# Kernel optimization log

Measured on AMD Instinct MI355X. Metric: run time of the kernel, lower is better.

The kernel has to match this reference:

```python
import jax, jax.numpy as jnp
import numpy as np

B, S, H, D = 8, 4096, 1024, 256  # batch, seq, hidden_size, state_size


def setup_inputs() -> dict:
    key = jax.random.key(0)
    ks = jax.random.split(key, 4)
    scale_in = 1.0 / np.sqrt(H)
    scale_st = 1.0 / np.sqrt(D)
    return {
        "x": jax.random.normal(ks[0], (B, S, H), dtype=jnp.float32),
        "W_in": jax.random.normal(ks[1], (H, D), dtype=jnp.float32) * scale_in,
        "b_in": jnp.zeros((D,), dtype=jnp.float32),
        "W_state": jax.random.normal(ks[2], (D, D), dtype=jnp.float32) * scale_st,
        "b_state": jnp.zeros((D,), dtype=jnp.float32),
        "W_out": jax.random.normal(ks[3], (D, H), dtype=jnp.float32) * scale_st,
        "b_out": jnp.zeros((H,), dtype=jnp.float32),
    }


def reference(x, W_in, b_in, W_state, b_state, W_out, b_out):
    # Precompute input projection for all timesteps in one big GEMM: [B,S,D]
    inp = jnp.einsum("bsh,hd->bsd", x, W_in) + b_in

    def step(state, inp_t):
        # state: [B,D], inp_t: [B,D]
        state = jnp.tanh(inp_t + state @ W_state + b_state)
        return state, state

    state0 = jnp.zeros((x.shape[0], W_state.shape[0]), dtype=x.dtype)
    # scan over time axis -> states: [S,B,D]
    _, states = jax.lax.scan(step, state0, jnp.swapaxes(inp, 0, 1))
    # output projection: [S,B,H] -> [B,S,H]
    out = jnp.einsum("sbd,dh->sbh", states, W_out) + b_out
    return jnp.swapaxes(out, 0, 1)
```

## Files before the change

### kernel.cpp

```cpp
#include <hip/hip_runtime.h>


typedef float v4f __attribute__((ext_vector_type(4)));
typedef __bf16 bf16x4 __attribute__((ext_vector_type(4)));
typedef __bf16 bf16x8 __attribute__((ext_vector_type(8)));
typedef _Float16 h8 __attribute__((ext_vector_type(8)));

#define BARRIER_LGKM() asm volatile("s_waitcnt lgkmcnt(0)\n\ts_barrier" ::: "memory")

__global__ void cvt_f32_bf16_x4(const float* __restrict__ in,
                                __bf16* __restrict__ out, int n4) {
  int i = blockIdx.x * blockDim.x + threadIdx.x;
  if (i >= n4) return;
  v4f v = ((const v4f*)in)[i];
  bf16x4 o;
  o.x = (__bf16)v.x; o.y = (__bf16)v.y; o.z = (__bf16)v.z; o.w = (__bf16)v.w;
  ((bf16x4*)out)[i] = o;
}

__global__ void transpose_cvt(const float* __restrict__ in,
                              __bf16* __restrict__ out, int K, int N) {
  int i = blockIdx.x * blockDim.x + threadIdx.x;
  if (i >= K * N) return;
  int k = i / N;
  int n = i - k * N;
  out[(size_t)n * K + k] = (__bf16)in[i];
}

__global__ void gemm_bt(const __bf16* __restrict__ A,
                        const __bf16* __restrict__ Bt,
                        const float* __restrict__ bias,
                        float* __restrict__ C,
                        int M, int N, int K) {
  int wid  = (blockIdx.x * blockDim.x + threadIdx.x) >> 6;
  int lane = threadIdx.x & 63;
  int ntiles = N >> 4;
  int mt = wid / ntiles;
  int nt = wid - mt * ntiles;
  if (mt * 16 >= M) return;
  int r = lane & 15;
  int q = lane >> 4;
  const __bf16* arow = A + (size_t)(mt * 16 + r) * K + q * 8;
  const __bf16* brow = Bt + (size_t)(nt * 16 + r) * K + q * 8;
  v4f acc = {0.f, 0.f, 0.f, 0.f};
  for (int k = 0; k < K; k += 32) {
    bf16x8 af = *(const bf16x8*)(arow + k);
    bf16x8 bf = *(const bf16x8*)(brow + k);
    acc = __builtin_amdgcn_mfma_f32_16x16x32_bf16(af, bf, acc, 0, 0, 0);
  }
  int col = nt * 16 + r;
  float bv = bias[col];
  size_t base = (size_t)(mt * 16 + q * 4) * N + col;
#pragma unroll
  for (int i = 0; i < 4; ++i) C[base + (size_t)i * N] = acc[i] + bv;
}

__global__ __launch_bounds__(256, 1) void scan_mfma(
    const float* __restrict__ inp,
    const float* __restrict__ Wst,
    const float* __restrict__ b_state,
    __bf16* __restrict__ states,
    int S) {
  const int tid = threadIdx.x;
  const int l = tid & 63;
  const int q = l >> 4;
  const int r = l & 15;
  const int w = tid >> 6;
  const int b = blockIdx.x;

  __shared__ __align__(16) _Float16 sbuf[2][256];

  h8 bw0[8], bw1[8], bw2[8], bw3[8];
#pragma unroll
  for (int c = 0; c < 8; ++c) {
#pragma unroll
    for (int i = 0; i < 8; ++i) {
      const float* wr = Wst + (size_t)(32 * c + 8 * q + i) * 256 + w * 64 + r;
      bw0[c][i] = (_Float16)wr[0];
      bw1[c][i] = (_Float16)wr[16];
      bw2[c][i] = (_Float16)wr[32];
      bw3[c][i] = (_Float16)wr[48];
    }
  }

  const float bst = b_state[tid];
  const float* inpb = inp + (size_t)b * S * 256;
  __bf16* stb = states + (size_t)b * S * 256;

  sbuf[0][tid] = (_Float16)0.f;
  float u_cur = inpb[tid];
  float u_nxt = inpb[256 + tid];
  __syncthreads();

  int cur = 0;
  for (int t = 0; t < S; ++t) {
    float u_n2 = 0.f;
    if (t + 2 < S) u_n2 = inpb[(size_t)(t + 2) * 256 + tid];

    const h8* sp = (const h8*)sbuf[cur];
    h8 af[8];
#pragma unroll
    for (int c = 0; c < 8; ++c) af[c] = sp[4 * c + q];

    v4f a0 = {0.f, 0.f, 0.f, 0.f};
    v4f a1 = a0, a2 = a0, a3 = a0;
#pragma unroll
    for (int c = 0; c < 8; ++c) {
      a0 = __builtin_amdgcn_mfma_f32_16x16x32_f16(af[c], bw0[c], a0, 0, 0, 0);
      a1 = __builtin_amdgcn_mfma_f32_16x16x32_f16(af[c], bw1[c], a1, 0, 0, 0);
      a2 = __builtin_amdgcn_mfma_f32_16x16x32_f16(af[c], bw2[c], a2, 0, 0, 0);
      a3 = __builtin_amdgcn_mfma_f32_16x16x32_f16(af[c], bw3[c], a3, 0, 0, 0);
    }
    float x = (q == 0) ? a0[0] : (q == 1) ? a1[0] : (q == 2) ? a2[0] : a3[0];
    x += u_cur + bst;

    float e = __expf(2.f * x);
    float sn = 1.f - 2.f * __builtin_amdgcn_rcpf(e + 1.f);

    cur ^= 1;
    sbuf[cur][tid] = (_Float16)sn;
    stb[(size_t)t * 256 + tid] = (__bf16)sn;
    u_cur = u_nxt;
    u_nxt = u_n2;
    BARRIER_LGKM();
  }
}

extern "C" void kernel_launch(void* const* d_in, const int* in_sizes, int n_in,
                              void* d_out, int out_size, void* d_ws,
                              size_t ws_size, hipStream_t stream) {
  const float* x       = (const float*)d_in[0];
  const float* W_in    = (const float*)d_in[1];
  const float* b_in    = (const float*)d_in[2];
  const float* W_state = (const float*)d_in[3];
  const float* b_state = (const float*)d_in[4];
  const float* W_out   = (const float*)d_in[5];
  const float* b_out   = (const float*)d_in[6];
  float* out = (float*)d_out;

  const int B = 8, S = 4096, H = 1024, D = 256;
  const int M = B * S;

  char* ws = (char*)d_ws;
  float*  inp    = (float*)(ws + 0);
  __bf16* states = (__bf16*)(ws + 33554432);
  __bf16* xb     = (__bf16*)(ws + 50331648);
  __bf16* WinT   = (__bf16*)(ws + 117440512);
  __bf16* WoutT  = (__bf16*)(ws + 117964800);

  cvt_f32_bf16_x4<<<(M * H / 4 + 255) / 256, 256, 0, stream>>>(x, xb, M * H / 4);
  transpose_cvt<<<(H * D + 255) / 256, 256, 0, stream>>>(W_in, WinT, H, D);
  transpose_cvt<<<(D * H + 255) / 256, 256, 0, stream>>>(W_out, WoutT, D, H);

  {
    int waves = (M / 16) * (D / 16);
    gemm_bt<<<waves / 4, 256, 0, stream>>>(xb, WinT, b_in, inp, M, D, H);
  }

  scan_mfma<<<B, 256, 0, stream>>>(inp, W_state, b_state, states, S);

  {
    int waves = (M / 16) * (H / 16);
    gemm_bt<<<waves / 4, 256, 0, stream>>>(states, WoutT, b_out, out, M, H, D);
  }
}
```

Baseline: 2.621 ms.

## Replace per-wave GEMM with LDS-tiled double-buffered 128x128 MFMA GEMM

The naive GEMM, where each wave computes one 16x16 tile straight from global memory, is replaced by a 128x128 block-tiled kernel. It stages A and B tiles into swizzled LDS using global_load_lds and double-buffers them across the K loop, so operands are reused across 16 MFMA accumulators per wave. The scan loop also gets small tweaks: pointer-increment addressing, an exp2f-based tanh, and removal of the t+2 bounds check. That last change reads past the end of each batch's input on the final steps, which still lands inside the workspace.

```diff
diff --git a/kernel.cpp b/kernel.cpp
--- a/kernel.cpp
+++ b/kernel.cpp
@@ -1,4 +1,5 @@
 #include <hip/hip_runtime.h>
+#include <stdint.h>
 
 
 typedef float v4f __attribute__((ext_vector_type(4)));
@@ -7,6 +8,11 @@
 typedef _Float16 h8 __attribute__((ext_vector_type(8)));
 
 #define BARRIER_LGKM() asm volatile("s_waitcnt lgkmcnt(0)\n\ts_barrier" ::: "memory")
+
+#define GLOAD_LDS16(g, l)                                                    \
+  __builtin_amdgcn_global_load_lds(                                          \
+      (const __attribute__((address_space(1))) void*)(g),                    \
+      (__attribute__((address_space(3))) void*)(l), 16, 0, 0)
 
 __global__ void cvt_f32_bf16_x4(const float* __restrict__ in,
                                 __bf16* __restrict__ out, int n4) {
@@ -27,32 +33,99 @@
   out[(size_t)n * K + k] = (__bf16)in[i];
 }
 
-__global__ void gemm_bt(const __bf16* __restrict__ A,
-                        const __bf16* __restrict__ Bt,
-                        const float* __restrict__ bias,
-                        float* __restrict__ C,
-                        int M, int N, int K) {
-  int wid  = (blockIdx.x * blockDim.x + threadIdx.x) >> 6;
-  int lane = threadIdx.x & 63;
-  int ntiles = N >> 4;
-  int mt = wid / ntiles;
-  int nt = wid - mt * ntiles;
-  if (mt * 16 >= M) return;
-  int r = lane & 15;
-  int q = lane >> 4;
-  const __bf16* arow = A + (size_t)(mt * 16 + r) * K + q * 8;
-  const __bf16* brow = Bt + (size_t)(nt * 16 + r) * K + q * 8;
-  v4f acc = {0.f, 0.f, 0.f, 0.f};
-  for (int k = 0; k < K; k += 32) {
-    bf16x8 af = *(const bf16x8*)(arow + k);
-    bf16x8 bf = *(const bf16x8*)(brow + k);
-    acc = __builtin_amdgcn_mfma_f32_16x16x32_bf16(af, bf, acc, 0, 0, 0);
-  }
-  int col = nt * 16 + r;
-  float bv = bias[col];
-  size_t base = (size_t)(mt * 16 + q * 4) * N + col;
-#pragma unroll
-  for (int i = 0; i < 4; ++i) C[base + (size_t)i * N] = acc[i] + bv;
+__global__ __launch_bounds__(256) void gemm_tile(
+    const __bf16* __restrict__ A,
+    const __bf16* __restrict__ Bt,
+    const float* __restrict__ bias,
+    float* __restrict__ C,
+    int M, int N, int K) {
+  const int tid = threadIdx.x;
+  const int lane = tid & 63;
+  const int w = tid >> 6;
+  const int wr = w >> 1, wc = w & 1;
+  const int r = lane & 15, q = lane >> 4;
+
+  const int nbn = N >> 7;
+  const int mb = blockIdx.x / nbn;
+  const int nb = blockIdx.x - mb * nbn;
+  const int m0 = mb << 7, n0 = nb << 7;
+
+  __shared__ __align__(16) char lds[2][16384];
+
+  const __bf16* gA[2];
+  const __bf16* gB[2];
+  int loff[2];
+#pragma unroll
+  for (int j = 0; j < 2; ++j) {
+    int o = (w * 2 + j) * 1024 + lane * 16;
+    int row = o >> 6;
+    int s = (o >> 4) & 3;
+    int ss = s ^ ((row >> 1) & 3);
+    gA[j] = A + (size_t)(m0 + row) * K + ss * 8;
+    gB[j] = Bt + (size_t)(n0 + row) * K + ss * 8;
+    loff[j] = (w * 2 + j) * 1024;
+  }
+
+  const int slot = (q ^ ((r >> 1) & 3)) * 16;
+  int aoff[4], boff[4];
+#pragma unroll
+  for (int i = 0; i < 4; ++i) {
+    aoff[i] = (wr * 64 + i * 16 + r) * 64 + slot;
+    boff[i] = 8192 + (wc * 64 + i * 16 + r) * 64 + slot;
+  }
+
+  v4f acc[4][4];
+#pragma unroll
+  for (int mi = 0; mi < 4; ++mi)
+#pragma unroll
+    for (int ni = 0; ni < 4; ++ni) acc[mi][ni] = (v4f){0.f, 0.f, 0.f, 0.f};
+
+  const int NK = K >> 5;
+#pragma unroll
+  for (int j = 0; j < 2; ++j) {
+    GLOAD_LDS16(gA[j], lds[0] + loff[j]);
+    GLOAD_LDS16(gB[j], lds[0] + 8192 + loff[j]);
+  }
+
+  for (int kt = 0; kt < NK; ++kt) {
+    __syncthreads();
+    if (kt + 1 < NK) {
+      const int b = (kt + 1) & 1;
+      const int ke = (kt + 1) * 32;
+#pragma unroll
+      for (int j = 0; j < 2; ++j) {
+        GLOAD_LDS16(gA[j] + ke, lds[b] + loff[j]);
+        GLOAD_LDS16(gB[j] + ke, lds[b] + 8192 + loff[j]);
+      }
+    }
+    const char* Lb = lds[kt & 1];
+    bf16x8 af[4], bf[4];
+#pragma unroll
+    for (int i = 0; i < 4; ++i) af[i] = *(const bf16x8*)(Lb + aoff[i]);
+#pragma unroll
+    for (int i = 0; i < 4; ++i) bf[i] = *(const bf16x8*)(Lb + boff[i]);
+#pragma unroll
+    for (int mi = 0; mi < 4; ++mi)
+#pragma unroll
+      for (int ni = 0; ni < 4; ++ni)
+        acc[mi][ni] = __builtin_amdgcn_mfma_f32_16x16x32_bf16(
+            af[mi], bf[ni], acc[mi][ni], 0, 0, 0);
+  }
+
+  float bv[4];
+#pragma unroll
+  for (int ni = 0; ni < 4; ++ni) bv[ni] = bias[n0 + wc * 64 + ni * 16 + r];
+#pragma unroll
+  for (int mi = 0; mi < 4; ++mi) {
+    int rowb = m0 + wr * 64 + mi * 16 + q * 4;
+#pragma unroll
+    for (int ni = 0; ni < 4; ++ni) {
+      int col = n0 + wc * 64 + ni * 16 + r;
+      float* cp = C + (size_t)rowb * N + col;
+#pragma unroll
+      for (int i = 0; i < 4; ++i) cp[(size_t)i * N] = acc[mi][ni][i] + bv[ni];
+    }
+  }
 }
 
 __global__ __launch_bounds__(256, 1) void scan_mfma(
@@ -75,11 +148,11 @@
   for (int c = 0; c < 8; ++c) {
 #pragma unroll
     for (int i = 0; i < 8; ++i) {
-      const float* wr = Wst + (size_t)(32 * c + 8 * q + i) * 256 + w * 64 + r;
-      bw0[c][i] = (_Float16)wr[0];
-      bw1[c][i] = (_Float16)wr[16];
-      bw2[c][i] = (_Float16)wr[32];
-      bw3[c][i] = (_Float16)wr[48];
+      const float* wr_ = Wst + (size_t)(32 * c + 8 * q + i) * 256 + w * 64 + r;
+      bw0[c][i] = (_Float16)wr_[0];
+      bw1[c][i] = (_Float16)wr_[16];
+      bw2[c][i] = (_Float16)wr_[32];
+      bw3[c][i] = (_Float16)wr_[48];
     }
   }
 
@@ -90,12 +163,14 @@
   sbuf[0][tid] = (_Float16)0.f;
   float u_cur = inpb[tid];
   float u_nxt = inpb[256 + tid];
+  const float* pin = inpb + 512;
+  __bf16* pst = stb;
   __syncthreads();
 
   int cur = 0;
   for (int t = 0; t < S; ++t) {
-    float u_n2 = 0.f;
-    if (t + 2 < S) u_n2 = inpb[(size_t)(t + 2) * 256 + tid];
+    float u_n2 = pin[tid];
+    pin += 256;
 
     const h8* sp = (const h8*)sbuf[cur];
     h8 af[8];
@@ -114,12 +189,13 @@
     float x = (q == 0) ? a0[0] : (q == 1) ? a1[0] : (q == 2) ? a2[0] : a3[0];
     x += u_cur + bst;
 
-    float e = __expf(2.f * x);
+    float e = exp2f(2.885390082f * x);
     float sn = 1.f - 2.f * __builtin_amdgcn_rcpf(e + 1.f);
 
     cur ^= 1;
     sbuf[cur][tid] = (_Float16)sn;
-    stb[(size_t)t * 256 + tid] = (__bf16)sn;
+    pst[tid] = (__bf16)sn;
+    pst += 256;
     u_cur = u_nxt;
     u_nxt = u_n2;
     BARRIER_LGKM();
@@ -152,15 +228,9 @@
   transpose_cvt<<<(H * D + 255) / 256, 256, 0, stream>>>(W_in, WinT, H, D);
   transpose_cvt<<<(D * H + 255) / 256, 256, 0, stream>>>(W_out, WoutT, D, H);
 
-  {
-    int waves = (M / 16) * (D / 16);
-    gemm_bt<<<waves / 4, 256, 0, stream>>>(xb, WinT, b_in, inp, M, D, H);
-  }
+  gemm_tile<<<(M / 128) * (D / 128), 256, 0, stream>>>(xb, WinT, b_in, inp, M, D, H);
 
   scan_mfma<<<B, 256, 0, stream>>>(inp, W_state, b_state, states, S);
 
-  {
-    int waves = (M / 16) * (H / 16);
-    gemm_bt<<<waves / 4, 256, 0, stream>>>(states, WoutT, b_out, out, M, H, D);
-  }
-}
+  gemm_tile<<<(M / 128) * (H / 128), 256, 0, stream>>>(states, WoutT, b_out, out, M, H, D);
+}
```

New measurement: 2.454 ms. 1.07x faster.
